# Performance work log

Measured on AMD Instinct MI355X. Metric: run time of the kernel, lower is better.

## Reference

```python
import jax, jax.numpy as jnp
import numpy as np

T, B, E, H = 1024, 8, 1024, 16
HD = E // H                       # 64
SCALE = float(HD * 1) ** -0.5     # scaling_factor = 1


def setup_inputs() -> dict:
    key = jax.random.key(0)
    ks = jax.random.split(key, 7)
    s = 0.02
    return {
        "query": jax.random.normal(ks[0], (T, B, E), jnp.float32),
        "key_padding_mask": jax.random.bernoulli(ks[1], 0.1, (B, T)),
        "attn_bias": jax.random.normal(ks[2], (1, H, T, T), jnp.float32) * 0.1,
        "wq": jax.random.normal(ks[3], (1, E, E), jnp.float32) * s,
        "wk": jax.random.normal(ks[4], (1, E, E), jnp.float32) * s,
        "wv": jax.random.normal(ks[5], (1, E, E), jnp.float32) * s,
        "wo": jax.random.normal(ks[6], (1, E, E), jnp.float32) * s,
    }


def _group_linear(x, w):
    # x: (T, B, nb*din), w: (nb, din, dout) -> (T, B, nb*dout). nb=1 here.
    t, b, _ = x.shape
    nb, din, dout = w.shape
    y = jnp.einsum('xnd,nde->xne', x.reshape(t * b, nb, din), w)
    return y.reshape(t, b, nb * dout)


def reference(query, key_padding_mask, attn_bias, wq, wk, wv, wo):
    q = _group_linear(query, wq) * SCALE
    k = _group_linear(query, wk)
    v = _group_linear(query, wv)

    # (T, B, E) -> (B*H, T, HD), matching torch view+transpose
    def split_heads(x):
        return x.reshape(T, B * H, HD).transpose(1, 0, 2)

    q, k, v = split_heads(q), split_heads(k), split_heads(v)

    scores = jnp.einsum('bth,bsh->bts', q, k).reshape(B, H, T, T)
    scores = scores + attn_bias
    scores = jnp.where(key_padding_mask[:, None, None, :], -jnp.inf, scores)
    probs = jax.nn.softmax(scores.astype(jnp.float32), axis=-1).astype(query.dtype)

    vh = v.reshape(B, H, T, HD)  # (B*H,T,HD) -> (B,H,S,HD)
    attn = jnp.einsum('bhts,bhsd->tbhd', probs, vh).reshape(T, B, H * HD)
    return _group_linear(attn, wo)
```

## Files before the change

### kernel.cpp

```cpp
#include <hip/hip_runtime.h>


typedef __bf16 bf16x8 __attribute__((ext_vector_type(8)));
typedef float f32x4 __attribute__((ext_vector_type(4)));

#define LOG2E 1.4426950408889634f
#define QSCALE 0.18033688011112042f

static __device__ __forceinline__ unsigned short f2bf_rn(float f) {
  union { float f; unsigned u; } x;
  x.f = f;
  unsigned r = (x.u + 0x7fffu + ((x.u >> 16) & 1u)) >> 16;
  return (unsigned short)r;
}
static __device__ __forceinline__ unsigned short f2bf(float f) {
  union { float f; unsigned u; } x;
  x.f = f;
  return (unsigned short)((x.u + 0x8000u) >> 16);
}

static __device__ __forceinline__ void async_cp16(const void* g, void* l) {
  __builtin_amdgcn_global_load_lds((__attribute__((address_space(1))) void*)g,
                                   (__attribute__((address_space(3))) void*)l,
                                   16, 0, 0);
}

__global__ __launch_bounds__(256, 2) void k_prep(
    const float* __restrict__ query, const int* __restrict__ mask,
    const float* __restrict__ bias,
    const float* __restrict__ wq, const float* __restrict__ wk,
    const float* __restrict__ wv, const float* __restrict__ wo,
    unsigned short* __restrict__ Abuf, float* __restrict__ Mfg,
    unsigned short* __restrict__ WqkvT, unsigned short* __restrict__ WoT,
    unsigned short* __restrict__ B2) {
  __shared__ char shraw[128 * 132 * 2];
  const int bid = blockIdx.x;
  const int tid = threadIdx.x;

  if (bid < 1024) {
    unsigned short* tile = (unsigned short*)shraw;
    const int ss = bid & 7, tt = (bid >> 3) & 7, h = bid >> 6;
    const float* src = bias + ((long)h * 1024 + tt * 128) * 1024 + ss * 128;
#pragma unroll
    for (int c = 0; c < 16; ++c) {
      int flat = c * 256 + tid;
      int row = flat >> 5, col = (flat & 31) << 2;
      float4 v = *(const float4*)(src + (long)row * 1024 + col);
      unsigned short* t4 = &tile[row * 132 + col];
      t4[0] = f2bf_rn(v.x * LOG2E); t4[1] = f2bf_rn(v.y * LOG2E);
      t4[2] = f2bf_rn(v.z * LOG2E); t4[3] = f2bf_rn(v.w * LOG2E);
    }
    __syncthreads();
    const int wid = tid >> 6, lane = tid & 63, lanelo = lane & 15, quad = lane >> 4;
    unsigned short outv[64];
#pragma unroll
    for (int mi = 0; mi < 2; ++mi)
#pragma unroll
      for (int nj = 0; nj < 8; ++nj)
#pragma unroll
        for (int r = 0; r < 4; ++r)
          outv[mi * 32 + nj * 4 + r] =
              tile[(wid * 32 + mi * 16 + quad * 4 + r) * 132 + nj * 16 + lanelo];
    unsigned short* dst = B2 + ((((long)(h * 8 + tt) * 8 + ss) * 256 + tid) << 6);
#pragma unroll
    for (int i = 0; i < 8; ++i) ((uint4*)dst)[i] = ((const uint4*)outv)[i];
  } else if (bid < 5120) {
    float (*tile)[33] = (float(*)[33])shraw;
    const int f = bid - 1024;
    const int bx = (f & 31) << 5;
    const int by = ((f >> 5) & 31) << 5;
    const int z = f >> 10;
    const float* src = (z == 0) ? wq : (z == 1) ? wk : (z == 2) ? wv : wo;
    unsigned short* dst = (z < 3) ? WqkvT + (size_t)z * 1024 * 1024 : WoT;
    const int tx = tid & 31, ty = tid >> 5;
#pragma unroll
    for (int i = 0; i < 32; i += 8)
      tile[ty + i][tx] = src[(size_t)(by + ty + i) * 1024 + bx + tx];
    __syncthreads();
#pragma unroll
    for (int i = 0; i < 32; i += 8)
      dst[(size_t)(bx + ty + i) * 1024 + by + tx] = f2bf_rn(tile[tx][ty + i]);
  } else if (bid < 13312) {
    const int idx = (bid - 5120) * 256 + tid;
    const float4 f = ((const float4*)query)[idx];
    unsigned lo = (unsigned)f2bf_rn(f.x) | ((unsigned)f2bf_rn(f.y) << 16);
    unsigned hi = (unsigned)f2bf_rn(f.z) | ((unsigned)f2bf_rn(f.w) << 16);
    uint2 v; v.x = lo; v.y = hi;
    *(uint2*)(Abuf + (size_t)idx * 4) = v;
  } else {
    const int i = (bid - 13312) * 256 + tid;
    Mfg[i] = mask[i] ? -1e30f : 0.f;
  }
}

static __device__ __forceinline__ void gemm_tile_128x128(
    const unsigned short* __restrict__ A, const unsigned short* __restrict__ Bt,
    int K, long m0, long n0,
    unsigned short* As, unsigned short* Bs, f32x4 acc[4][4]) {
  const int tid = threadIdx.x;
  const int wid = tid >> 6;
  const int lane = tid & 63;
  const int lanelo = lane & 15;
  const int quad = lane >> 4;
  const int wm = (wid >> 1) << 6;
  const int wn = (wid & 1) << 6;
  const int srow = tid >> 3;
  const int scol = (((tid & 7) ^ (srow & 7)) << 3);

  for (int k0 = 0; k0 < K; k0 += 64) {
    __syncthreads();
    {
      char* la = (char*)As + (wid << 10);
      char* lb = (char*)Bs + (wid << 10);
#pragma unroll
      for (int c = 0; c < 4; ++c) {
        const unsigned short* ga = A + (m0 + srow + c * 32) * K + k0 + scol;
        const unsigned short* gb = Bt + (n0 + srow + c * 32) * K + k0 + scol;
        async_cp16(ga, la + c * 4096);
        async_cp16(gb, lb + c * 4096);
      }
    }
    __syncthreads();
#pragma unroll
    for (int kk = 0; kk < 2; ++kk) {
      bf16x8 a[4], b[4];
#pragma unroll
      for (int i = 0; i < 4; ++i) {
        const int ra = wm + i * 16 + lanelo;
        const int rb = wn + i * 16 + lanelo;
        a[i] = *(const bf16x8*)(As + ra * 64 + (((kk * 4 + quad) ^ (ra & 7)) << 3));
        b[i] = *(const bf16x8*)(Bs + rb * 64 + (((kk * 4 + quad) ^ (rb & 7)) << 3));
      }
#pragma unroll
      for (int i = 0; i < 4; ++i)
#pragma unroll
        for (int j = 0; j < 4; ++j)
          acc[i][j] = __builtin_amdgcn_mfma_f32_16x16x32_bf16(a[i], b[j], acc[i][j], 0, 0, 0);
    }
  }
}

__global__ __launch_bounds__(256, 2) void k_gemm_qkv(
    const unsigned short* __restrict__ A, const unsigned short* __restrict__ Bt,
    unsigned short* __restrict__ Qh, unsigned short* __restrict__ Kh,
    unsigned short* __restrict__ Vt) {
  __shared__ unsigned short smem[16384];
  unsigned short* As = smem;
  unsigned short* Bs = smem + 8192;
  f32x4 acc[4][4];
  const f32x4 z4 = {0.f, 0.f, 0.f, 0.f};
#pragma unroll
  for (int i = 0; i < 4; ++i)
#pragma unroll
    for (int j = 0; j < 4; ++j) acc[i][j] = z4;

  const int flat = blockIdx.y * 24 + blockIdx.x;
  const int swz = (flat & 7) * 192 + (flat >> 3);
  const int bx = swz % 24, by = swz / 24;
  const long m0 = (long)by * 128;
  const long n0 = (long)bx * 128;
  gemm_tile_128x128(A, Bt, 1024, m0, n0, As, Bs, acc);

  const int tid = threadIdx.x;
  const int wid = tid >> 6;
  const int lane = tid & 63;
  const int lanelo = lane & 15;
  const int quad = lane >> 4;
  const int wm = (wid >> 1) << 6;
  const int wn = (wid & 1) << 6;
  const int which = bx >> 3;

  if (which == 2) {
    unsigned short* Vt_s = smem;
    const long t0g = m0 >> 3;
#pragma unroll
    for (int half = 0; half < 2; ++half) {
      __syncthreads();
      if ((wid & 1) == half) {
#pragma unroll
        for (int mi = 0; mi < 4; ++mi)
#pragma unroll
          for (int nj = 0; nj < 4; ++nj)
#pragma unroll
            for (int r = 0; r < 4; ++r)
              Vt_s[(wm + mi * 16 + quad * 4 + r) * 72 + nj * 16 + lanelo] =
                  f2bf(acc[mi][nj][r]);
      }
      __syncthreads();
      const int h = (((int)(n0 & 1023)) >> 6) + half;
#pragma unroll
      for (int pp = 0; pp < 2; ++pp) {
        int p = tid + pp * 256;
        int b = p >> 6, d = p & 63;
        long off = ((long)(b * 16 + h)) << 16;
        __attribute__((aligned(16))) unsigned short vals[16];
#pragma unroll
        for (int t = 0; t < 16; ++t) vals[t] = Vt_s[(t * 8 + b) * 72 + d];
        uint4* dst = (uint4*)(Vt + off + (long)d * 1024 + t0g);
        dst[0] = ((const uint4*)vals)[0];
        dst[1] = ((const uint4*)vals)[1];
      }
    }
  } else {
#pragma unroll
    for (int mi = 0; mi < 4; ++mi)
#pragma unroll
      for (int nj = 0; nj < 4; ++nj)
#pragma unroll
        for (int r = 0; r < 4; ++r) {
          int m = (int)m0 + wm + mi * 16 + quad * 4 + r;
          int n = (int)n0 + wn + nj * 16 + lanelo;
          float v = acc[mi][nj][r];
          int t = m >> 3, b = m & 7;
          int e = n & 1023, h = e >> 6, d = e & 63;
          long off = ((long)(b * 16 + h)) << 16;
          if (which == 0)
            Qh[off + t * 64 + d] = f2bf(v * QSCALE);
          else
            Kh[off + t * 64 + d] = f2bf(v);
        }
  }
}

__global__ __launch_bounds__(512, 4) void k_attn(
    const unsigned short* __restrict__ Qh, const unsigned short* __restrict__ Kh,
    const unsigned short* __restrict__ Vt, const unsigned short* __restrict__ B2,
    const float* __restrict__ Mfg, unsigned short* __restrict__ A2) {
  __shared__ unsigned short Ks[128 * 72];
  __shared__ unsigned short Vs[64 * 136];
  __shared__ unsigned short Ps[128 * 72];

  const int tid = threadIdx.x;
  const int wid = tid >> 6;
  const int lane = tid & 63;
  const int lanelo = lane & 15;
  const int quad = lane >> 4;
  const int bh = blockIdx.x;
  const int b = bh >> 4, h = bh & 15;
  const int tt = blockIdx.y;
  const int t0 = tt * 128;
  const long head = (long)bh << 16;

  bf16x8 aq[2];
#pragma unroll
  for (int ks = 0; ks < 2; ++ks)
    aq[ks] = *(const bf16x8*)(Qh + head +
                              (long)(t0 + wid * 16 + lanelo) * 64 +
                              ks * 32 + quad * 8);

  const f32x4 z4 = {0.f, 0.f, 0.f, 0.f};
  f32x4 Oacc[4];
#pragma unroll
  for (int dj = 0; dj < 4; ++dj) Oacc[dj] = z4;
  float mrow[4], lrow[4];
#pragma unroll
  for (int r = 0; r < 4; ++r) { mrow[r] = -1e30f; lrow[r] = 0.f; }

  const long biasbase = (((long)(h * 8 + tt) * 8) * 256 + (wid >> 1) * 64 + lane) * 64 +
                        (wid & 1) * 32;

  for (int s0 = 0; s0 < 1024; s0 += 128) {
    bf16x8 bfr[4];
    {
      const bf16x8* bp8 = (const bf16x8*)(B2 + biasbase + ((long)(s0 >> 7) * 256 << 6));
#pragma unroll
      for (int i = 0; i < 4; ++i) bfr[i] = bp8[i];
    }
    float madd[8];
#pragma unroll
    for (int nj = 0; nj < 8; ++nj)
      madd[nj] = Mfg[(long)b * 1024 + s0 + nj * 16 + lanelo];

    __syncthreads();
#pragma unroll
    for (int c = 0; c < 2; ++c) {
      int flat = c * 4096 + tid * 8;
      int row = flat >> 6, col = flat & 63;
      uint4 v = *(const uint4*)(Kh + head + (long)(s0 + row) * 64 + col);
      *(uint4*)&Ks[row * 72 + col] = v;
    }
#pragma unroll
    for (int c = 0; c < 2; ++c) {
      int flat = c * 4096 + tid * 8;
      int row = flat >> 7, col = flat & 127;
      uint4 v = *(const uint4*)(Vt + head + (long)row * 1024 + s0 + col);
      *(uint4*)&Vs[row * 136 + col] = v;
    }
    __syncthreads();

    f32x4 S[8];
#pragma unroll
    for (int nj = 0; nj < 8; ++nj)
#pragma unroll
      for (int r = 0; r < 4; ++r)
        S[nj][r] = (float)bfr[nj >> 1][(nj & 1) * 4 + r] + madd[nj];

#pragma unroll
    for (int ks = 0; ks < 2; ++ks) {
      bf16x8 bk[8];
#pragma unroll
      for (int nj = 0; nj < 8; ++nj)
        bk[nj] = *(const bf16x8*)(Ks + (nj * 16 + lanelo) * 72 + ks * 32 + quad * 8);
#pragma unroll
      for (int nj = 0; nj < 8; ++nj)
        S[nj] = __builtin_amdgcn_mfma_f32_16x16x32_bf16(aq[ks], bk[nj], S[nj], 0, 0, 0);
    }

#pragma unroll
    for (int r = 0; r < 4; ++r) {
      float mx = S[0][r];
#pragma unroll
      for (int nj = 1; nj < 8; ++nj) mx = fmaxf(mx, S[nj][r]);
      mx = fmaxf(mx, __shfl_xor(mx, 1, 16));
      mx = fmaxf(mx, __shfl_xor(mx, 2, 16));
      mx = fmaxf(mx, __shfl_xor(mx, 4, 16));
      mx = fmaxf(mx, __shfl_xor(mx, 8, 16));
      float mold = mrow[r];
      float mnew = fmaxf(mold, mx);
      float al = exp2f(mold - mnew);
      mrow[r] = mnew;
      float rs = 0.f;
#pragma unroll
      for (int nj = 0; nj < 8; ++nj) {
        float p = exp2f(S[nj][r] - mnew);
        S[nj][r] = p;
        rs += p;
      }
      rs += __shfl_xor(rs, 1, 16);
      rs += __shfl_xor(rs, 2, 16);
      rs += __shfl_xor(rs, 4, 16);
      rs += __shfl_xor(rs, 8, 16);
      lrow[r] = lrow[r] * al + rs;
#pragma unroll
      for (int dj = 0; dj < 4; ++dj) Oacc[dj][r] *= al;
    }

#pragma unroll
    for (int half = 0; half < 2; ++half) {
#pragma unroll
      for (int njl = 0; njl < 4; ++njl)
#pragma unroll
        for (int r = 0; r < 4; ++r)
          Ps[(wid * 16 + quad * 4 + r) * 72 + njl * 16 + lanelo] =
              f2bf(S[half * 4 + njl][r]);
#pragma unroll
      for (int ks2 = 0; ks2 < 2; ++ks2) {
        const int ks = half * 2 + ks2;
        bf16x8 ap, bv[4];
        ap = *(const bf16x8*)(Ps + (wid * 16 + lanelo) * 72 + ks2 * 32 + quad * 8);
#pragma unroll
        for (int dj = 0; dj < 4; ++dj)
          bv[dj] = *(const bf16x8*)(Vs + (dj * 16 + lanelo) * 136 + ks * 32 + quad * 8);
#pragma unroll
        for (int dj = 0; dj < 4; ++dj)
          Oacc[dj] = __builtin_amdgcn_mfma_f32_16x16x32_bf16(ap, bv[dj], Oacc[dj], 0, 0, 0);
      }
    }
  }

#pragma unroll
  for (int r = 0; r < 4; ++r) {
    float rinv = __builtin_amdgcn_rcpf(lrow[r]);
    int t = t0 + wid * 16 + quad * 4 + r;
#pragma unroll
    for (int dj = 0; dj < 4; ++dj) {
      int d = dj * 16 + lanelo;
      A2[(long)(t * 8 + b) * 1024 + h * 64 + d] = f2bf(Oacc[dj][r] * rinv);
    }
  }
}

__global__ __launch_bounds__(256, 2) void k_gemm_out(
    const unsigned short* __restrict__ A, const unsigned short* __restrict__ Bt,
    float* __restrict__ out) {
  __shared__ unsigned short As[128 * 64];
  __shared__ unsigned short Bs[128 * 64];
  f32x4 acc[4][4];
  const f32x4 z4 = {0.f, 0.f, 0.f, 0.f};
#pragma unroll
  for (int i = 0; i < 4; ++i)
#pragma unroll
    for (int j = 0; j < 4; ++j) acc[i][j] = z4;

  const int flat = blockIdx.y * 8 + blockIdx.x;
  const int swz = (flat & 7) * 64 + (flat >> 3);
  const long m0 = (long)(swz / 8) * 128;
  const long n0 = (long)(swz % 8) * 128;
  gemm_tile_128x128(A, Bt, 1024, m0, n0, As, Bs, acc);

  const int tid = threadIdx.x;
  const int wid = tid >> 6;
  const int lane = tid & 63;
  const int lanelo = lane & 15;
  const int quad = lane >> 4;
  const int wm = (wid >> 1) << 6;
  const int wn = (wid & 1) << 6;
#pragma unroll
  for (int mi = 0; mi < 4; ++mi)
#pragma unroll
    for (int nj = 0; nj < 4; ++nj)
#pragma unroll
      for (int r = 0; r < 4; ++r) {
        long m = m0 + wm + mi * 16 + quad * 4 + r;
        long n = n0 + wn + nj * 16 + lanelo;
        out[m * 1024 + n] = acc[mi][nj][r];
      }
}

extern "C" void kernel_launch(void* const* d_in, const int* in_sizes, int n_in,
                              void* d_out, int out_size, void* d_ws, size_t ws_size,
                              hipStream_t stream) {
  const float* query = (const float*)d_in[0];
  const int* mask = (const int*)d_in[1];
  const float* bias = (const float*)d_in[2];
  const float* wq = (const float*)d_in[3];
  const float* wk = (const float*)d_in[4];
  const float* wv = (const float*)d_in[5];
  const float* wo = (const float*)d_in[6];
  float* out = (float*)d_out;

  char* ws = (char*)d_ws;
  const size_t MB = 1024 * 1024;
  unsigned short* Abuf  = (unsigned short*)(ws);
  unsigned short* WqkvT = (unsigned short*)(ws + 16 * MB);
  unsigned short* WoT   = (unsigned short*)(ws + 22 * MB);
  unsigned short* Qh    = (unsigned short*)(ws + 24 * MB);
  unsigned short* Kh    = (unsigned short*)(ws + 40 * MB);
  unsigned short* Vt    = (unsigned short*)(ws + 56 * MB);
  unsigned short* A2    = (unsigned short*)(ws + 72 * MB);
  unsigned short* B2    = (unsigned short*)(ws + 88 * MB);
  float*          Mfg   = (float*)(ws + 120 * MB);

  k_prep<<<dim3(13344), dim3(256), 0, stream>>>(query, mask, bias, wq, wk, wv, wo,
                                                Abuf, Mfg, WqkvT, WoT, B2);
  k_gemm_qkv<<<dim3(24, 64), dim3(256), 0, stream>>>(Abuf, WqkvT, Qh, Kh, Vt);
  k_attn<<<dim3(128, 8), dim3(512), 0, stream>>>(Qh, Kh, Vt, B2, Mfg, A2);
  k_gemm_out<<<dim3(8, 64), dim3(256), 0, stream>>>(A2, WoT, out);
}
```

Before: 356.2 us.

## Double-buffer LDS tiles in shared GEMM to overlap global loads with MFMA

The shared 128x128 GEMM tile loop now keeps two LDS buffers per operand. It issues the async global-to-LDS copies for the next K slice before computing on the current one, replacing the two barriers per iteration with one wait plus barrier at the end. This aims to hide global memory latency behind the MFMA work in the QKV and output projection GEMMs. LDS use per block doubles to 64 KB, which may cut occupancy below the two blocks per CU that the launch bounds request.

Result: no change. 362.1 us (+1.7%).

```diff
diff --git a/kernel.cpp b/kernel.cpp
--- a/kernel.cpp
+++ b/kernel.cpp
@@ -107,20 +107,39 @@
   const int srow = tid >> 3;
   const int scol = (((tid & 7) ^ (srow & 7)) << 3);
 
-  for (int k0 = 0; k0 < K; k0 += 64) {
-    __syncthreads();
-    {
-      char* la = (char*)As + (wid << 10);
-      char* lb = (char*)Bs + (wid << 10);
+  const unsigned short* ga0 = A + (m0 + srow) * K + scol;
+  const unsigned short* gb0 = Bt + (n0 + srow) * K + scol;
+
+  {
+    char* la = (char*)As + (wid << 10);
+    char* lb = (char*)Bs + (wid << 10);
+#pragma unroll
+    for (int c = 0; c < 4; ++c) {
+      async_cp16(ga0 + (long)c * 32 * K, la + c * 4096);
+      async_cp16(gb0 + (long)c * 32 * K, lb + c * 4096);
+    }
+  }
+  asm volatile("s_waitcnt vmcnt(0)" ::: "memory");
+  __builtin_amdgcn_s_barrier();
+  __builtin_amdgcn_sched_barrier(0);
+
+  const int nt = K >> 6;
+  for (int t = 0; t < nt; ++t) {
+    const int curb = (t & 1) << 14;
+    if (t + 1 < nt) {
+      const int nxtb = ((t + 1) & 1) << 14;
+      char* la = (char*)As + nxtb + (wid << 10);
+      char* lb = (char*)Bs + nxtb + (wid << 10);
+      const unsigned short* ga = ga0 + (t + 1) * 64;
+      const unsigned short* gb = gb0 + (t + 1) * 64;
 #pragma unroll
       for (int c = 0; c < 4; ++c) {
-        const unsigned short* ga = A + (m0 + srow + c * 32) * K + k0 + scol;
-        const unsigned short* gb = Bt + (n0 + srow + c * 32) * K + k0 + scol;
-        async_cp16(ga, la + c * 4096);
-        async_cp16(gb, lb + c * 4096);
-      }
-    }
-    __syncthreads();
+        async_cp16(ga + (long)c * 32 * K, la + c * 4096);
+        async_cp16(gb + (long)c * 32 * K, lb + c * 4096);
+      }
+    }
+    const unsigned short* Asb = (const unsigned short*)((const char*)As + curb);
+    const unsigned short* Bsb = (const unsigned short*)((const char*)Bs + curb);
 #pragma unroll
     for (int kk = 0; kk < 2; ++kk) {
       bf16x8 a[4], b[4];
@@ -128,8 +147,8 @@
       for (int i = 0; i < 4; ++i) {
         const int ra = wm + i * 16 + lanelo;
         const int rb = wn + i * 16 + lanelo;
-        a[i] = *(const bf16x8*)(As + ra * 64 + (((kk * 4 + quad) ^ (ra & 7)) << 3));
-        b[i] = *(const bf16x8*)(Bs + rb * 64 + (((kk * 4 + quad) ^ (rb & 7)) << 3));
+        a[i] = *(const bf16x8*)(Asb + ra * 64 + (((kk * 4 + quad) ^ (ra & 7)) << 3));
+        b[i] = *(const bf16x8*)(Bsb + rb * 64 + (((kk * 4 + quad) ^ (rb & 7)) << 3));
       }
 #pragma unroll
       for (int i = 0; i < 4; ++i)
@@ -137,6 +156,9 @@
         for (int j = 0; j < 4; ++j)
           acc[i][j] = __builtin_amdgcn_mfma_f32_16x16x32_bf16(a[i], b[j], acc[i][j], 0, 0, 0);
     }
+    asm volatile("s_waitcnt vmcnt(0) lgkmcnt(0)" ::: "memory");
+    __builtin_amdgcn_s_barrier();
+    __builtin_amdgcn_sched_barrier(0);
   }
 }
 
@@ -144,9 +166,9 @@
     const unsigned short* __restrict__ A, const unsigned short* __restrict__ Bt,
     unsigned short* __restrict__ Qh, unsigned short* __restrict__ Kh,
     unsigned short* __restrict__ Vt) {
-  __shared__ unsigned short smem[16384];
+  __shared__ unsigned short smem[32768];
   unsigned short* As = smem;
-  unsigned short* Bs = smem + 8192;
+  unsigned short* Bs = smem + 16384;
   f32x4 acc[4][4];
   const f32x4 z4 = {0.f, 0.f, 0.f, 0.f};
 #pragma unroll
@@ -373,8 +395,8 @@
 __global__ __launch_bounds__(256, 2) void k_gemm_out(
     const unsigned short* __restrict__ A, const unsigned short* __restrict__ Bt,
     float* __restrict__ out) {
-  __shared__ unsigned short As[128 * 64];
-  __shared__ unsigned short Bs[128 * 64];
+  __shared__ unsigned short As[16384];
+  __shared__ unsigned short Bs[16384];
   f32x4 acc[4][4];
   const f32x4 z4 = {0.f, 0.f, 0.f, 0.f};
 #pragma unroll
```

## Split QKV GEMM into pipelined 256x256 QK kernel and separate V kernel

Applied to the files above, without the earlier changes.

Replaces the fused QKV projection GEMM with two kernels. A new 512-thread kernel computes Q and K using 256x256 tiles, an 8-slot async LDS ring buffer, explicit waitcnt/barrier scheduling and MFMA priority boosts. The V projection keeps the old 128x128 path with its transposed store. The goal is more data reuse and better load/compute overlap on the larger Q/K part, at the cost of an extra kernel launch, 128KB of LDS per block and fewer blocks in flight.

Result: no change. 350.5 us (-1.6%).

```diff
diff --git a/kernel.cpp b/kernel.cpp
--- a/kernel.cpp
+++ b/kernel.cpp
@@ -93,6 +93,211 @@
   }
 }
 
+__global__ __launch_bounds__(512, 2) void k_gemm_qk(
+    const unsigned short* __restrict__ A, const unsigned short* __restrict__ Bt,
+    unsigned short* __restrict__ Qh, unsigned short* __restrict__ Kh) {
+  __shared__ unsigned short smem[65536];
+
+  const int tid = threadIdx.x;
+  const int wid = tid >> 6;
+  const int lane = tid & 63;
+  const int lanelo = lane & 15;
+  const int quad = lane >> 4;
+  const int wm = (wid >> 2) << 7;
+  const int wn = (wid & 3) << 6;
+  const int K = 1024;
+
+  const int flat = blockIdx.y * 8 + blockIdx.x;
+  const int swz = (flat & 7) * 32 + (flat >> 3);
+  const int bx = swz & 7, by = swz >> 3;
+  const long m0 = (long)by * 256;
+  const long n0 = (long)bx * 256;
+
+  const int x_ = (tid & 7) ^ ((tid >> 3) & 7);
+  const int row_s = ((tid >> 3) << 1) + (x_ >> 2);
+  const int col_s = (x_ & 3) << 3;
+  const unsigned short* gA = A + (m0 + row_s) * K + col_s;
+  const unsigned short* gB = Bt + (n0 + row_s) * K + col_s;
+
+#define STG(slot, gp, kc)                                        \
+  do {                                                           \
+    const unsigned short* _g = (gp) + (kc);                      \
+    char* _l = (char*)smem + ((slot) << 14) + (wid << 10);       \
+    async_cp16(_g, _l);                                          \
+    async_cp16(_g + 128 * 1024, _l + 8192);                      \
+  } while (0)
+
+  const int lhalf = lanelo >> 1;
+  const int posa = ((((lanelo & 1) << 2) + quad) ^ lhalf) << 3;
+  const int aoff = ((wm >> 1) + lhalf) * 64 + posa;
+  const int boff = ((wn >> 1) + lhalf) * 64 + posa;
+
+  bf16x8 a[4], b[4];
+#define LDA4(slot, mb)                                                        \
+  do {                                                                        \
+    a[0] = *(const bf16x8*)(smem + (slot) * 8192 + aoff + ((mb) + 0) * 512);  \
+    a[1] = *(const bf16x8*)(smem + (slot) * 8192 + aoff + ((mb) + 1) * 512);  \
+    a[2] = *(const bf16x8*)(smem + (slot) * 8192 + aoff + ((mb) + 2) * 512);  \
+    a[3] = *(const bf16x8*)(smem + (slot) * 8192 + aoff + ((mb) + 3) * 512);  \
+  } while (0)
+#define LDB4(slot)                                                            \
+  do {                                                                        \
+    b[0] = *(const bf16x8*)(smem + (slot) * 8192 + boff + 0 * 512);           \
+    b[1] = *(const bf16x8*)(smem + (slot) * 8192 + boff + 1 * 512);           \
+    b[2] = *(const bf16x8*)(smem + (slot) * 8192 + boff + 2 * 512);           \
+    b[3] = *(const bf16x8*)(smem + (slot) * 8192 + boff + 3 * 512);           \
+  } while (0)
+
+  f32x4 acc[8][4];
+  const f32x4 z4 = {0.f, 0.f, 0.f, 0.f};
+#pragma unroll
+  for (int i = 0; i < 8; ++i)
+#pragma unroll
+    for (int j = 0; j < 4; ++j) acc[i][j] = z4;
+
+#define MMA16(mb)                                                             \
+  do {                                                                        \
+    __builtin_amdgcn_s_setprio(1);                                            \
+    _Pragma("unroll") for (int x = 0; x < 4; ++x)                             \
+        _Pragma("unroll") for (int y = 0; y < 4; ++y)                         \
+        acc[(mb) + x][y] = __builtin_amdgcn_mfma_f32_16x16x32_bf16(           \
+            a[x], b[y], acc[(mb) + x][y], 0, 0, 0);                           \
+    __builtin_amdgcn_s_setprio(0);                                            \
+  } while (0)
+
+#define BARSYNC()                                                             \
+  do {                                                                        \
+    __builtin_amdgcn_s_barrier();                                             \
+    __builtin_amdgcn_sched_barrier(0);                                        \
+  } while (0)
+
+  STG(2, gB, 0);
+  STG(0, gA, 0);
+  STG(3, gB, 32);
+  STG(1, gA, 32);
+  STG(6, gB, 64);
+  STG(4, gA, 64);
+  STG(7, gB, 96);
+  asm volatile("s_waitcnt vmcnt(6)" ::: "memory");
+  BARSYNC();
+
+#pragma unroll 1
+  for (int i = 0; i < 7; ++i) {
+    const int kc1 = i * 128 + 96;
+    const int kc2 = i * 128 + 128;
+    const int kc3 = i * 128 + 192;
+    LDA4(0, 0);
+    LDB4(2);
+    STG(5, gA, kc1);
+    BARSYNC();
+    MMA16(0);
+    BARSYNC();
+    LDA4(0, 4);
+    STG(2, gB, kc2);
+    BARSYNC();
+    MMA16(4);
+    BARSYNC();
+    LDA4(1, 0);
+    LDB4(3);
+    STG(0, gA, kc2);
+    BARSYNC();
+    MMA16(0);
+    BARSYNC();
+    LDA4(1, 4);
+    STG(3, gB, kc2 + 32);
+    BARSYNC();
+    MMA16(4);
+    asm volatile("s_waitcnt vmcnt(6)" ::: "memory");
+    BARSYNC();
+    LDA4(4, 0);
+    LDB4(6);
+    STG(1, gA, kc2 + 32);
+    BARSYNC();
+    MMA16(0);
+    BARSYNC();
+    LDA4(4, 4);
+    STG(6, gB, kc3);
+    BARSYNC();
+    MMA16(4);
+    BARSYNC();
+    LDA4(5, 0);
+    LDB4(7);
+    STG(4, gA, kc3);
+    BARSYNC();
+    MMA16(0);
+    BARSYNC();
+    LDA4(5, 4);
+    STG(7, gB, kc3 + 32);
+    BARSYNC();
+    MMA16(4);
+    asm volatile("s_waitcnt vmcnt(6)" ::: "memory");
+    BARSYNC();
+  }
+  {
+    LDA4(0, 0);
+    LDB4(2);
+    STG(5, gA, 7 * 128 + 96);
+    BARSYNC();
+    MMA16(0);
+    BARSYNC();
+    LDA4(0, 4);
+    BARSYNC();
+    MMA16(4);
+    BARSYNC();
+    LDA4(1, 0);
+    LDB4(3);
+    BARSYNC();
+    MMA16(0);
+    BARSYNC();
+    LDA4(1, 4);
+    BARSYNC();
+    MMA16(4);
+    asm volatile("s_waitcnt vmcnt(0)" ::: "memory");
+    BARSYNC();
+    LDA4(4, 0);
+    LDB4(6);
+    BARSYNC();
+    MMA16(0);
+    BARSYNC();
+    LDA4(4, 4);
+    BARSYNC();
+    MMA16(4);
+    BARSYNC();
+    LDA4(5, 0);
+    LDB4(7);
+    BARSYNC();
+    MMA16(0);
+    BARSYNC();
+    LDA4(5, 4);
+    BARSYNC();
+    MMA16(4);
+  }
+#undef STG
+#undef LDA4
+#undef LDB4
+#undef MMA16
+#undef BARSYNC
+
+  const int which = bx >> 2;
+#pragma unroll
+  for (int mi = 0; mi < 8; ++mi)
+#pragma unroll
+    for (int nj = 0; nj < 4; ++nj)
+#pragma unroll
+      for (int r = 0; r < 4; ++r) {
+        int m = (int)m0 + wm + mi * 16 + quad * 4 + r;
+        int n = (int)n0 + wn + nj * 16 + lanelo;
+        float v = acc[mi][nj][r];
+        int t = m >> 3, bb = m & 7;
+        int e = n & 1023, h = e >> 6, d = e & 63;
+        long off = ((long)(bb * 16 + h)) << 16;
+        if (which == 0)
+          Qh[off + t * 64 + d] = f2bf(v * QSCALE);
+        else
+          Kh[off + t * 64 + d] = f2bf(v);
+      }
+}
+
 static __device__ __forceinline__ void gemm_tile_128x128(
     const unsigned short* __restrict__ A, const unsigned short* __restrict__ Bt,
     int K, long m0, long n0,
@@ -140,9 +345,8 @@
   }
 }
 
-__global__ __launch_bounds__(256, 2) void k_gemm_qkv(
+__global__ __launch_bounds__(256, 2) void k_gemm_v(
     const unsigned short* __restrict__ A, const unsigned short* __restrict__ Bt,
-    unsigned short* __restrict__ Qh, unsigned short* __restrict__ Kh,
     unsigned short* __restrict__ Vt) {
   __shared__ unsigned short smem[16384];
   unsigned short* As = smem;
@@ -154,11 +358,10 @@
 #pragma unroll
     for (int j = 0; j < 4; ++j) acc[i][j] = z4;
 
-  const int flat = blockIdx.y * 24 + blockIdx.x;
-  const int swz = (flat & 7) * 192 + (flat >> 3);
-  const int bx = swz % 24, by = swz / 24;
-  const long m0 = (long)by * 128;
-  const long n0 = (long)bx * 128;
+  const int flat = blockIdx.y * 8 + blockIdx.x;
+  const int swz = (flat & 7) * 64 + (flat >> 3);
+  const long m0 = (long)(swz / 8) * 128;
+  const long n0 = 2048 + (long)(swz % 8) * 128;
   gemm_tile_128x128(A, Bt, 1024, m0, n0, As, Bs, acc);
 
   const int tid = threadIdx.x;
@@ -168,57 +371,36 @@
   const int quad = lane >> 4;
   const int wm = (wid >> 1) << 6;
   const int wn = (wid & 1) << 6;
-  const int which = bx >> 3;
-
-  if (which == 2) {
-    unsigned short* Vt_s = smem;
-    const long t0g = m0 >> 3;
-#pragma unroll
-    for (int half = 0; half < 2; ++half) {
-      __syncthreads();
-      if ((wid & 1) == half) {
-#pragma unroll
-        for (int mi = 0; mi < 4; ++mi)
-#pragma unroll
-          for (int nj = 0; nj < 4; ++nj)
-#pragma unroll
-            for (int r = 0; r < 4; ++r)
-              Vt_s[(wm + mi * 16 + quad * 4 + r) * 72 + nj * 16 + lanelo] =
-                  f2bf(acc[mi][nj][r]);
-      }
-      __syncthreads();
-      const int h = (((int)(n0 & 1023)) >> 6) + half;
-#pragma unroll
-      for (int pp = 0; pp < 2; ++pp) {
-        int p = tid + pp * 256;
-        int b = p >> 6, d = p & 63;
-        long off = ((long)(b * 16 + h)) << 16;
-        __attribute__((aligned(16))) unsigned short vals[16];
-#pragma unroll
-        for (int t = 0; t < 16; ++t) vals[t] = Vt_s[(t * 8 + b) * 72 + d];
-        uint4* dst = (uint4*)(Vt + off + (long)d * 1024 + t0g);
-        dst[0] = ((const uint4*)vals)[0];
-        dst[1] = ((const uint4*)vals)[1];
-      }
-    }
-  } else {
-#pragma unroll
-    for (int mi = 0; mi < 4; ++mi)
-#pragma unroll
-      for (int nj = 0; nj < 4; ++nj)
-#pragma unroll
-        for (int r = 0; r < 4; ++r) {
-          int m = (int)m0 + wm + mi * 16 + quad * 4 + r;
-          int n = (int)n0 + wn + nj * 16 + lanelo;
-          float v = acc[mi][nj][r];
-          int t = m >> 3, b = m & 7;
-          int e = n & 1023, h = e >> 6, d = e & 63;
-          long off = ((long)(b * 16 + h)) << 16;
-          if (which == 0)
-            Qh[off + t * 64 + d] = f2bf(v * QSCALE);
-          else
-            Kh[off + t * 64 + d] = f2bf(v);
-        }
+
+  unsigned short* Vt_s = smem;
+  const long t0g = m0 >> 3;
+#pragma unroll
+  for (int half = 0; half < 2; ++half) {
+    __syncthreads();
+    if ((wid & 1) == half) {
+#pragma unroll
+      for (int mi = 0; mi < 4; ++mi)
+#pragma unroll
+        for (int nj = 0; nj < 4; ++nj)
+#pragma unroll
+          for (int r = 0; r < 4; ++r)
+            Vt_s[(wm + mi * 16 + quad * 4 + r) * 72 + nj * 16 + lanelo] =
+                f2bf(acc[mi][nj][r]);
+    }
+    __syncthreads();
+    const int h = (((int)(n0 & 1023)) >> 6) + half;
+#pragma unroll
+    for (int pp = 0; pp < 2; ++pp) {
+      int p = tid + pp * 256;
+      int b = p >> 6, d = p & 63;
+      long off = ((long)(b * 16 + h)) << 16;
+      __attribute__((aligned(16))) unsigned short vals[16];
+#pragma unroll
+      for (int t = 0; t < 16; ++t) vals[t] = Vt_s[(t * 8 + b) * 72 + d];
+      uint4* dst = (uint4*)(Vt + off + (long)d * 1024 + t0g);
+      dst[0] = ((const uint4*)vals)[0];
+      dst[1] = ((const uint4*)vals)[1];
+    }
   }
 }
 
@@ -433,7 +615,8 @@
 
   k_prep<<<dim3(13344), dim3(256), 0, stream>>>(query, mask, bias, wq, wk, wv, wo,
                                                 Abuf, Mfg, WqkvT, WoT, B2);
-  k_gemm_qkv<<<dim3(24, 64), dim3(256), 0, stream>>>(Abuf, WqkvT, Qh, Kh, Vt);
+  k_gemm_qk<<<dim3(8, 32), dim3(512), 0, stream>>>(Abuf, WqkvT, Qh, Kh);
+  k_gemm_v<<<dim3(8, 64), dim3(256), 0, stream>>>(Abuf, WqkvT, Vt);
   k_attn<<<dim3(128, 8), dim3(512), 0, stream>>>(Qh, Kh, Vt, B2, Mfg, A2);
   k_gemm_out<<<dim3(8, 64), dim3(256), 0, stream>>>(A2, WoT, out);
 }
```
